# Kernel optimization log

Hardware: AMD Instinct MI355X
Metric: run time of the kernel (lower is better)

The kernel has to match this reference:

```python
import jax, jax.numpy as jnp
import numpy as np

N, M = 8192, 8192
N_POS, N_NEG = 2_000_000, 8_000_000


def setup_inputs() -> dict:
    key = jax.random.key(0)
    k1, k2, k3, k4, k5, k6, k7 = jax.random.split(key, 7)
    return {
        "drug_protein_reconstruct": jax.random.normal(k1, (N, M), dtype=jnp.float32),
        "drug_protein": jax.random.uniform(k2, (N, M), dtype=jnp.float32),
        "alpha": jax.random.uniform(k3, (1,), dtype=jnp.float32),
        "pos_x_index": jax.random.randint(k4, (N_POS,), 0, N, dtype=jnp.int64 if jax.config.jax_enable_x64 else jnp.int32),
        "pos_y_index": jax.random.randint(k5, (N_POS,), 0, M, dtype=jnp.int64 if jax.config.jax_enable_x64 else jnp.int32),
        "neg_x_index": jax.random.randint(k6, (N_NEG,), 0, N, dtype=jnp.int64 if jax.config.jax_enable_x64 else jnp.int32),
        "neg_y_index": jax.random.randint(k7, (N_NEG,), 0, M, dtype=jnp.int64 if jax.config.jax_enable_x64 else jnp.int32),
    }


def reference(drug_protein_reconstruct, drug_protein, alpha,
              pos_x_index, pos_y_index, neg_x_index, neg_y_index):
    # Fused gather -> subtract -> square -> sum (equivalent to dense MSE matrix
    # followed by fancy indexing, but without materializing the full loss_mat).
    a = alpha[0]
    pos_diff = (drug_protein_reconstruct[pos_x_index, pos_y_index]
                - drug_protein[pos_x_index, pos_y_index])
    neg_diff = (drug_protein_reconstruct[neg_x_index, neg_y_index]
                - drug_protein[neg_x_index, neg_y_index])
    pos_sum = jnp.sum(pos_diff * pos_diff)
    neg_sum = jnp.sum(neg_diff * neg_diff)
    return pos_sum * ((1.0 - a) * 0.5) + neg_sum * (a * 0.5)
```

## Files before the change

### kernel.cpp

```cpp
#include <hip/hip_runtime.h>

#define BLOCK 256
#define GRID 2048
#define ILP 4

typedef int v4i __attribute__((ext_vector_type(4)));

__global__ __launch_bounds__(BLOCK) void dti_pu_loss_kernel(
    const float* __restrict__ R,
    const float* __restrict__ D,
    const float* __restrict__ alpha,
    const int* __restrict__ px, const int* __restrict__ py, int npos,
    const int* __restrict__ nx, const int* __restrict__ ny, int nneg,
    float* __restrict__ out)
{
    const int tid    = blockIdx.x * BLOCK + threadIdx.x;
    const int stride = GRID * BLOCK;

    float pos_acc = 0.0f;
    float neg_acc = 0.0f;

    {
        const int n4 = npos >> 2;
        const v4i* px4 = (const v4i*)px;
        const v4i* py4 = (const v4i*)py;
        for (int base = tid * ILP; base < n4; base += stride * ILP) {
            v4i X[ILP], Y[ILP];
            #pragma unroll
            for (int k = 0; k < ILP; ++k) {
                if (base + k < n4) {
                    X[k] = __builtin_nontemporal_load(&px4[base + k]);
                    Y[k] = __builtin_nontemporal_load(&py4[base + k]);
                }
            }
            #pragma unroll
            for (int k = 0; k < ILP; ++k) {
                if (base + k < n4) {
                    int o0 = (X[k].x << 13) + Y[k].x;
                    int o1 = (X[k].y << 13) + Y[k].y;
                    int o2 = (X[k].z << 13) + Y[k].z;
                    int o3 = (X[k].w << 13) + Y[k].w;
                    float d0 = R[o0] - D[o0];
                    float d1 = R[o1] - D[o1];
                    float d2 = R[o2] - D[o2];
                    float d3 = R[o3] - D[o3];
                    pos_acc += d0 * d0 + d1 * d1 + d2 * d2 + d3 * d3;
                }
            }
        }
        for (int i = (n4 << 2) + tid; i < npos; i += stride) {
            int o = (px[i] << 13) + py[i];
            float d = R[o] - D[o];
            pos_acc += d * d;
        }
    }

    {
        const int n4 = nneg >> 2;
        const v4i* nx4 = (const v4i*)nx;
        const v4i* ny4 = (const v4i*)ny;
        for (int base = tid * ILP; base < n4; base += stride * ILP) {
            v4i X[ILP], Y[ILP];
            #pragma unroll
            for (int k = 0; k < ILP; ++k) {
                if (base + k < n4) {
                    X[k] = __builtin_nontemporal_load(&nx4[base + k]);
                    Y[k] = __builtin_nontemporal_load(&ny4[base + k]);
                }
            }
            #pragma unroll
            for (int k = 0; k < ILP; ++k) {
                if (base + k < n4) {
                    int o0 = (X[k].x << 13) + Y[k].x;
                    int o1 = (X[k].y << 13) + Y[k].y;
                    int o2 = (X[k].z << 13) + Y[k].z;
                    int o3 = (X[k].w << 13) + Y[k].w;
                    float d0 = R[o0] - D[o0];
                    float d1 = R[o1] - D[o1];
                    float d2 = R[o2] - D[o2];
                    float d3 = R[o3] - D[o3];
                    neg_acc += d0 * d0 + d1 * d1 + d2 * d2 + d3 * d3;
                }
            }
        }
        for (int i = (n4 << 2) + tid; i < nneg; i += stride) {
            int o = (nx[i] << 13) + ny[i];
            float d = R[o] - D[o];
            neg_acc += d * d;
        }
    }

    const float a = alpha[0];
    float v = pos_acc * ((1.0f - a) * 0.5f) + neg_acc * (a * 0.5f);

    #pragma unroll
    for (int off = 32; off > 0; off >>= 1)
        v += __shfl_down(v, off, 64);

    __shared__ float sdata[BLOCK / 64];
    const int lane = threadIdx.x & 63;
    const int wave = threadIdx.x >> 6;
    if (lane == 0) sdata[wave] = v;
    __syncthreads();
    if (threadIdx.x == 0) {
        float s = 0.0f;
        #pragma unroll
        for (int w = 0; w < BLOCK / 64; ++w) s += sdata[w];
        atomicAdd(out, s);
    }
}

extern "C" void kernel_launch(void* const* d_in, const int* in_sizes, int n_in,
                              void* d_out, int out_size, void* d_ws, size_t ws_size,
                              hipStream_t stream) {
    const float* R     = (const float*)d_in[0];
    const float* D     = (const float*)d_in[1];
    const float* alpha = (const float*)d_in[2];
    const int*   px    = (const int*)d_in[3];
    const int*   py    = (const int*)d_in[4];
    const int*   nx    = (const int*)d_in[5];
    const int*   ny    = (const int*)d_in[6];
    const int    npos  = in_sizes[3];
    const int    nneg  = in_sizes[5];

    float* out = (float*)d_out;

    hipMemsetAsync(out, 0, sizeof(float), stream);

    dti_pu_loss_kernel<<<GRID, BLOCK, 0, stream>>>(
        R, D, alpha, px, py, npos, nx, ny, nneg, out);
}
```

Measured before the change: 844.1 us.

## Bucket gather indices by row range and route buckets to XCDs for L2 locality

Adds a partition pass that packs each (x, y, pos/neg) index into a 32-bit word and scatters it into 256 buckets keyed by high row bits, using shared-memory counting and global atomic bases. A second pass assigns bucket subsets to each XCD by blockIdx mod 8, so each XCD's L2 serves a narrower slice of R and D. The aim is to cut the cost of random 4-byte gathers over two 256 MB matrices by improving cache-line reuse. In exchange it adds a full write and re-read of the packed indices plus atomics, and falls back to a direct kernel when the workspace is too small.

```diff
diff --git a/kernel.cpp b/kernel.cpp
--- a/kernel.cpp
+++ b/kernel.cpp
@@ -1,102 +1,20 @@
 #include <hip/hip_runtime.h>
 
 #define BLOCK 256
-#define GRID 2048
-#define ILP 4
+#define GRID  2048
+#define NBUCK 256
+#define PIPT  16
+#define PCHUNK (BLOCK * PIPT)
 
 typedef int v4i __attribute__((ext_vector_type(4)));
 
-__global__ __launch_bounds__(BLOCK) void dti_pu_loss_kernel(
-    const float* __restrict__ R,
-    const float* __restrict__ D,
-    const float* __restrict__ alpha,
-    const int* __restrict__ px, const int* __restrict__ py, int npos,
-    const int* __restrict__ nx, const int* __restrict__ ny, int nneg,
-    float* __restrict__ out)
-{
-    const int tid    = blockIdx.x * BLOCK + threadIdx.x;
-    const int stride = GRID * BLOCK;
-
-    float pos_acc = 0.0f;
-    float neg_acc = 0.0f;
-
-    {
-        const int n4 = npos >> 2;
-        const v4i* px4 = (const v4i*)px;
-        const v4i* py4 = (const v4i*)py;
-        for (int base = tid * ILP; base < n4; base += stride * ILP) {
-            v4i X[ILP], Y[ILP];
-            #pragma unroll
-            for (int k = 0; k < ILP; ++k) {
-                if (base + k < n4) {
-                    X[k] = __builtin_nontemporal_load(&px4[base + k]);
-                    Y[k] = __builtin_nontemporal_load(&py4[base + k]);
-                }
-            }
-            #pragma unroll
-            for (int k = 0; k < ILP; ++k) {
-                if (base + k < n4) {
-                    int o0 = (X[k].x << 13) + Y[k].x;
-                    int o1 = (X[k].y << 13) + Y[k].y;
-                    int o2 = (X[k].z << 13) + Y[k].z;
-                    int o3 = (X[k].w << 13) + Y[k].w;
-                    float d0 = R[o0] - D[o0];
-                    float d1 = R[o1] - D[o1];
-                    float d2 = R[o2] - D[o2];
-                    float d3 = R[o3] - D[o3];
-                    pos_acc += d0 * d0 + d1 * d1 + d2 * d2 + d3 * d3;
-                }
-            }
-        }
-        for (int i = (n4 << 2) + tid; i < npos; i += stride) {
-            int o = (px[i] << 13) + py[i];
-            float d = R[o] - D[o];
-            pos_acc += d * d;
-        }
-    }
-
-    {
-        const int n4 = nneg >> 2;
-        const v4i* nx4 = (const v4i*)nx;
-        const v4i* ny4 = (const v4i*)ny;
-        for (int base = tid * ILP; base < n4; base += stride * ILP) {
-            v4i X[ILP], Y[ILP];
-            #pragma unroll
-            for (int k = 0; k < ILP; ++k) {
-                if (base + k < n4) {
-                    X[k] = __builtin_nontemporal_load(&nx4[base + k]);
-                    Y[k] = __builtin_nontemporal_load(&ny4[base + k]);
-                }
-            }
-            #pragma unroll
-            for (int k = 0; k < ILP; ++k) {
-                if (base + k < n4) {
-                    int o0 = (X[k].x << 13) + Y[k].x;
-                    int o1 = (X[k].y << 13) + Y[k].y;
-                    int o2 = (X[k].z << 13) + Y[k].z;
-                    int o3 = (X[k].w << 13) + Y[k].w;
-                    float d0 = R[o0] - D[o0];
-                    float d1 = R[o1] - D[o1];
-                    float d2 = R[o2] - D[o2];
-                    float d3 = R[o3] - D[o3];
-                    neg_acc += d0 * d0 + d1 * d1 + d2 * d2 + d3 * d3;
-                }
-            }
-        }
-        for (int i = (n4 << 2) + tid; i < nneg; i += stride) {
-            int o = (nx[i] << 13) + ny[i];
-            float d = R[o] - D[o];
-            neg_acc += d * d;
-        }
-    }
-
+__device__ __forceinline__ void block_reduce_out(float pos_acc, float neg_acc,
+                                                 const float* alpha, float* out) {
     const float a = alpha[0];
     float v = pos_acc * ((1.0f - a) * 0.5f) + neg_acc * (a * 0.5f);
-
     #pragma unroll
     for (int off = 32; off > 0; off >>= 1)
         v += __shfl_down(v, off, 64);
-
     __shared__ float sdata[BLOCK / 64];
     const int lane = threadIdx.x & 63;
     const int wave = threadIdx.x >> 6;
@@ -106,8 +24,173 @@
         float s = 0.0f;
         #pragma unroll
         for (int w = 0; w < BLOCK / 64; ++w) s += sdata[w];
-        atomicAdd(out, s);
-    }
+        if (s != 0.0f) atomicAdd(out, s);
+    }
+}
+
+__global__ __launch_bounds__(BLOCK) void partition_kernel(
+    const int* __restrict__ px, const int* __restrict__ py, int npos,
+    const int* __restrict__ nx, const int* __restrict__ ny, int nneg,
+    unsigned* __restrict__ items, unsigned* __restrict__ gcnt, int cap,
+    const float* __restrict__ R, const float* __restrict__ D,
+    const float* __restrict__ alpha, float* __restrict__ out)
+{
+    __shared__ unsigned s_cnt[NBUCK];
+    __shared__ unsigned s_base[NBUCK];
+    __shared__ unsigned s_cur[NBUCK];
+
+    const int tid   = threadIdx.x;
+    const int total = npos + nneg;
+    const int nchunks = (total + PCHUNK - 1) / PCHUNK;
+
+    float pos_acc = 0.0f, neg_acc = 0.0f;
+
+    for (int c = blockIdx.x; c < nchunks; c += gridDim.x) {
+        const int run = c * PCHUNK + tid * PIPT;
+        const int nval = min(PIPT, max(0, total - run));
+
+        unsigned it[PIPT];
+        if (nval == PIPT && run + PIPT <= npos) {
+            const v4i* x4 = (const v4i*)(px + run);
+            const v4i* y4 = (const v4i*)(py + run);
+            #pragma unroll
+            for (int q = 0; q < PIPT / 4; ++q) {
+                v4i xs = x4[q], ys = y4[q];
+                it[q*4+0] = ((unsigned)xs.x << 13) | (unsigned)ys.x;
+                it[q*4+1] = ((unsigned)xs.y << 13) | (unsigned)ys.y;
+                it[q*4+2] = ((unsigned)xs.z << 13) | (unsigned)ys.z;
+                it[q*4+3] = ((unsigned)xs.w << 13) | (unsigned)ys.w;
+            }
+        } else if (nval == PIPT && run >= npos && (((run - npos) & 3) == 0)) {
+            const int j = run - npos;
+            const v4i* x4 = (const v4i*)(nx + j);
+            const v4i* y4 = (const v4i*)(ny + j);
+            #pragma unroll
+            for (int q = 0; q < PIPT / 4; ++q) {
+                v4i xs = x4[q], ys = y4[q];
+                it[q*4+0] = (((unsigned)xs.x << 13) | (unsigned)ys.x) | (1u << 26);
+                it[q*4+1] = (((unsigned)xs.y << 13) | (unsigned)ys.y) | (1u << 26);
+                it[q*4+2] = (((unsigned)xs.z << 13) | (unsigned)ys.z) | (1u << 26);
+                it[q*4+3] = (((unsigned)xs.w << 13) | (unsigned)ys.w) | (1u << 26);
+            }
+        } else {
+            for (int k = 0; k < PIPT; ++k) {
+                const int gi = run + k;
+                if (k < nval) {
+                    if (gi < npos) it[k] = ((unsigned)px[gi] << 13) | (unsigned)py[gi];
+                    else {
+                        const int j = gi - npos;
+                        it[k] = (((unsigned)nx[j] << 13) | (unsigned)ny[j]) | (1u << 26);
+                    }
+                } else it[k] = 0;
+            }
+        }
+
+        s_cnt[tid] = 0;
+        __syncthreads();
+        #pragma unroll
+        for (int k = 0; k < PIPT; ++k)
+            if (k < nval) atomicAdd(&s_cnt[(it[k] >> 18) & 0xFF], 1u);
+        __syncthreads();
+
+        const unsigned cnt = s_cnt[tid];
+        if (cnt) s_base[tid] = atomicAdd(&gcnt[tid], cnt);
+        s_cur[tid] = 0;
+        __syncthreads();
+
+        #pragma unroll
+        for (int k = 0; k < PIPT; ++k) {
+            if (k < nval) {
+                const unsigned b = (it[k] >> 18) & 0xFF;
+                const unsigned p = atomicAdd(&s_cur[b], 1u);
+                const unsigned gpos = s_base[b] + p;
+                if (gpos < (unsigned)cap) {
+                    items[(size_t)b * cap + gpos] = it[k];
+                } else {
+                    const unsigned o = it[k] & 0x3FFFFFFu;
+                    const float d = R[o] - D[o];
+                    if (it[k] >> 26) neg_acc += d * d; else pos_acc += d * d;
+                }
+            }
+        }
+        __syncthreads();
+    }
+
+    block_reduce_out(pos_acc, neg_acc, alpha, out);
+}
+
+__global__ __launch_bounds__(BLOCK) void gather_kernel(
+    const float* __restrict__ R, const float* __restrict__ D,
+    const float* __restrict__ alpha,
+    const unsigned* __restrict__ items, const unsigned* __restrict__ gcnt,
+    int cap, float* __restrict__ out)
+{
+    const int xcd = blockIdx.x & 7;
+    const int g   = blockIdx.x >> 3;
+    const unsigned team_stride = (GRID / 8) * BLOCK;
+
+    float pos_acc = 0.0f, neg_acc = 0.0f;
+
+    for (int bi = 0; bi < NBUCK / 8; ++bi) {
+        const int b = bi * 8 + xcd;
+        const unsigned n = min(gcnt[b], (unsigned)cap);
+        const unsigned* ib = items + (size_t)b * cap;
+        for (unsigned i = (unsigned)g * BLOCK + threadIdx.x; i < n; i += team_stride) {
+            const unsigned it = ib[i];
+            const unsigned o = it & 0x3FFFFFFu;
+            const float d = R[o] - D[o];
+            if (it >> 26) neg_acc += d * d; else pos_acc += d * d;
+        }
+    }
+
+    block_reduce_out(pos_acc, neg_acc, alpha, out);
+}
+
+__global__ __launch_bounds__(BLOCK) void dti_direct_kernel(
+    const float* __restrict__ R, const float* __restrict__ D,
+    const float* __restrict__ alpha,
+    const int* __restrict__ px, const int* __restrict__ py, int npos,
+    const int* __restrict__ nx, const int* __restrict__ ny, int nneg,
+    float* __restrict__ out)
+{
+    const int tid = blockIdx.x * BLOCK + threadIdx.x;
+    const int stride = gridDim.x * BLOCK;
+    float pos_acc = 0.0f, neg_acc = 0.0f;
+    {
+        const int n4 = npos >> 2;
+        const v4i* px4 = (const v4i*)px;
+        const v4i* py4 = (const v4i*)py;
+        for (int i = tid; i < n4; i += stride) {
+            v4i xs = px4[i], ys = py4[i];
+            int o0 = (xs.x << 13) + ys.x, o1 = (xs.y << 13) + ys.y;
+            int o2 = (xs.z << 13) + ys.z, o3 = (xs.w << 13) + ys.w;
+            float d0 = R[o0]-D[o0], d1 = R[o1]-D[o1], d2 = R[o2]-D[o2], d3 = R[o3]-D[o3];
+            pos_acc += d0*d0 + d1*d1 + d2*d2 + d3*d3;
+        }
+        for (int i = (n4 << 2) + tid; i < npos; i += stride) {
+            int o = (px[i] << 13) + py[i];
+            float d = R[o] - D[o];
+            pos_acc += d * d;
+        }
+    }
+    {
+        const int n4 = nneg >> 2;
+        const v4i* nx4 = (const v4i*)nx;
+        const v4i* ny4 = (const v4i*)ny;
+        for (int i = tid; i < n4; i += stride) {
+            v4i xs = nx4[i], ys = ny4[i];
+            int o0 = (xs.x << 13) + ys.x, o1 = (xs.y << 13) + ys.y;
+            int o2 = (xs.z << 13) + ys.z, o3 = (xs.w << 13) + ys.w;
+            float d0 = R[o0]-D[o0], d1 = R[o1]-D[o1], d2 = R[o2]-D[o2], d3 = R[o3]-D[o3];
+            neg_acc += d0*d0 + d1*d1 + d2*d2 + d3*d3;
+        }
+        for (int i = (n4 << 2) + tid; i < nneg; i += stride) {
+            int o = (nx[i] << 13) + ny[i];
+            float d = R[o] - D[o];
+            neg_acc += d * d;
+        }
+    }
+    block_reduce_out(pos_acc, neg_acc, alpha, out);
 }
 
 extern "C" void kernel_launch(void* const* d_in, const int* in_sizes, int n_in,
@@ -122,11 +205,24 @@
     const int*   ny    = (const int*)d_in[6];
     const int    npos  = in_sizes[3];
     const int    nneg  = in_sizes[5];
+    const int    total = npos + nneg;
 
     float* out = (float*)d_out;
-
     hipMemsetAsync(out, 0, sizeof(float), stream);
 
-    dti_pu_loss_kernel<<<GRID, BLOCK, 0, stream>>>(
-        R, D, alpha, px, py, npos, nx, ny, nneg, out);
-}
+    const int cap = total / NBUCK + total / (NBUCK * 4) + 1024;
+    const size_t need = (size_t)NBUCK * cap * sizeof(unsigned) + NBUCK * sizeof(unsigned);
+
+    if (d_ws != nullptr && ws_size >= need) {
+        unsigned* items = (unsigned*)d_ws;
+        unsigned* gcnt  = items + (size_t)NBUCK * cap;
+        hipMemsetAsync(gcnt, 0, NBUCK * sizeof(unsigned), stream);
+        partition_kernel<<<GRID, BLOCK, 0, stream>>>(
+            px, py, npos, nx, ny, nneg, items, gcnt, cap, R, D, alpha, out);
+        gather_kernel<<<GRID, BLOCK, 0, stream>>>(
+            R, D, alpha, items, gcnt, cap, out);
+    } else {
+        dti_direct_kernel<<<GRID, BLOCK, 0, stream>>>(
+            R, D, alpha, px, py, npos, nx, ny, nneg, out);
+    }
+}
```

Result: faster. 708.1 us (-16.1%).
